# Kernel optimization log

Hardware: AMD Instinct MI355X
Metric: run time of the kernel (lower is better)

The kernel has to match this reference:

```python
import jax, jax.numpy as jnp
import numpy as np

VOCAB, E, H = 64, 256, 1024
B, T = 128, 512
RATE = 0.2  # self.dropout; note: input_dropout on int token ids is a no-op here (see notes)


def _dropout(key, x, rate):
    keep = jax.random.bernoulli(key, 1.0 - rate, x.shape)
    return jnp.where(keep, x / (1.0 - rate), jnp.zeros((), x.dtype))


def _lstm_dir(x, mask, Wx, Wh, b, reverse):
    # x: [B,T,E], mask: [B,T] bool. Keras LSTM gate order i,f,g,o.
    if reverse:
        x = jnp.flip(x, 1)
        mask = jnp.flip(mask, 1)
    xz = jnp.einsum('bte,eg->btg', x, Wx) + b          # [B,T,4H] input projection, one big GEMM
    h0 = jnp.zeros((x.shape[0], Wh.shape[0]), x.dtype)
    c0 = jnp.zeros_like(h0)

    def step(carry, inp):
        h, c = carry
        xz_t, m = inp                                   # [B,4H], [B,1] bool
        z = xz_t + h @ Wh
        i, f, g, o = jnp.split(z, 4, axis=-1)
        c_new = jax.nn.sigmoid(f) * c + jax.nn.sigmoid(i) * jnp.tanh(g)
        h_new = jax.nn.sigmoid(o) * jnp.tanh(c_new)
        h = jnp.where(m, h_new, h)                      # freeze state past row length
        c = jnp.where(m, c_new, c)
        return (h, c), jnp.where(m, h, jnp.zeros((), h.dtype))

    xs = (jnp.swapaxes(xz, 0, 1), jnp.swapaxes(mask, 0, 1)[..., None])
    _, ys = jax.lax.scan(step, (h0, c0), xs)            # ys: [T,B,H]
    ys = jnp.swapaxes(ys, 0, 1)
    if reverse:
        ys = jnp.flip(ys, 1)
    return ys


def setup_inputs() -> dict:
    key = jax.random.key(0)
    ks = jax.random.split(key, 9)
    tokens = jax.random.randint(ks[0], (B, T), 0, VOCAB, dtype=jnp.int32)
    lengths = jax.random.randint(ks[1], (B,), T // 2, T + 1, dtype=jnp.int32)
    emb = jax.random.normal(ks[2], (VOCAB, E), jnp.float32)
    sE, sH = 1.0 / np.sqrt(E), 1.0 / np.sqrt(H)
    Wx_f = jax.random.normal(ks[3], (E, 4 * H), jnp.float32) * sE
    Wh_f = jax.random.normal(ks[4], (H, 4 * H), jnp.float32) * sH
    b_f = jax.random.normal(ks[5], (4 * H,), jnp.float32) * 0.02
    Wx_b = jax.random.normal(ks[6], (E, 4 * H), jnp.float32) * sE
    Wh_b = jax.random.normal(ks[7], (H, 4 * H), jnp.float32) * sH
    b_b = jax.random.normal(ks[8], (4 * H,), jnp.float32) * 0.02
    return {"tokens": tokens, "lengths": lengths, "emb": emb,
            "Wx_f": Wx_f, "Wh_f": Wh_f, "b_f": b_f,
            "Wx_b": Wx_b, "Wh_b": Wh_b, "b_b": b_b}


def reference(tokens, lengths, emb, Wx_f, Wh_f, b_f, Wx_b, Wh_b, b_b):
    mask = jnp.arange(T, dtype=jnp.int32)[None, :] < lengths[:, None]  # [B,T]
    x = jnp.take(emb, tokens, axis=0)                                  # [B,T,E]
    x = _dropout(jax.random.key(1), x, RATE)                           # dropout on embedded
    x = jnp.where(mask[..., None], x, jnp.zeros((), x.dtype))
    out_f = _lstm_dir(x, mask, Wx_f, Wh_f, b_f, reverse=False)
    out_b = _lstm_dir(x, mask, Wx_b, Wh_b, b_b, reverse=True)
    out = out_f + out_b                                                # Bidirectional merge_mode='sum'
    out = _dropout(jax.random.key(2), out, RATE)                       # output dropout
    out = jnp.where(mask[..., None], out, jnp.zeros((), out.dtype))
    return out
```

## Files before the change

kernel.cpp:

```cpp
#include <hip/hip_runtime.h>
#include <hip/hip_bf16.h>

#define B_ 128
#define T_ 512
#define E_ 256
#define H_ 1024
#define G_ 4096
#define KTOT 1280

typedef _Float16 f16x8 __attribute__((ext_vector_type(8)));
typedef float f32x4 __attribute__((ext_vector_type(4)));

__device__ __forceinline__ void threefry2x32(unsigned k0, unsigned k1,
                                             unsigned x0, unsigned x1,
                                             unsigned& o0, unsigned& o1) {
  unsigned k2 = k0 ^ k1 ^ 0x1BD11BDAu;
  unsigned v0 = x0 + k0, v1 = x1 + k1;
#define RND(r) { v0 += v1; v1 = (v1 << (r)) | (v1 >> (32 - (r))); v1 ^= v0; }
  RND(13) RND(15) RND(26) RND(6)   v0 += k1; v1 += k2 + 1u;
  RND(17) RND(29) RND(16) RND(24)  v0 += k2; v1 += k0 + 2u;
  RND(13) RND(15) RND(26) RND(6)   v0 += k0; v1 += k1 + 3u;
  RND(17) RND(29) RND(16) RND(24)  v0 += k1; v1 += k2 + 4u;
  RND(13) RND(15) RND(26) RND(6)   v0 += k2; v1 += k0 + 5u;
#undef RND
  o0 = v0; o1 = v1;
}

__device__ __forceinline__ bool jax_keep(unsigned k1, unsigned i) {
  unsigned o0, o1;
  threefry2x32(0u, k1, 0u, i, o0, o1);
  unsigned bits = o0 ^ o1;
  float u = __uint_as_float((bits >> 9) | 0x3F800000u) - 1.0f;
  return u < 0.8f;
}

__global__ void embed_kernel(const int* __restrict__ tokens,
                             const int* __restrict__ lengths,
                             const float* __restrict__ emb,
                             _Float16* __restrict__ x) {
  unsigned i = blockIdx.x * 256u + threadIdx.x;
  if (i >= (unsigned)(B_ * T_ * E_)) return;
  int e = (int)(i & (E_ - 1));
  int t = (int)((i >> 8) & (T_ - 1));
  int b = (int)(i >> 17);
  int tok = tokens[b * T_ + t];
  float v = emb[tok * E_ + e];
  bool m = t < lengths[b];
  float xv = (m && jax_keep(1u, i)) ? (v * 1.25f) : 0.0f;
  x[i] = (_Float16)xv;
}

__device__ __forceinline__ float sigm(float v) { return 1.0f / (1.0f + __expf(-v)); }
__device__ __forceinline__ float tanh_fast(float v) {
  float c = fminf(fmaxf(v, -10.f), 10.f);
  float e = __expf(2.0f * c);
  return (e - 1.0f) / (e + 1.0f);
}

#define HLD(dst, base, OFF) \
  asm volatile("global_load_dwordx4 %0, %1, off offset:" OFF " sc0 sc1" \
               : "=v"(dst) : "v"(base))
#define HST2(addr, val) \
  asm volatile("global_store_short %0, %1, off sc0 sc1" :: "v"(addr), "v"(val))

#define HEAT() do { \
    _Pragma("unroll") \
    for (int z_ = 0; z_ < 8; ++z_) { \
      hx0 = __builtin_fmaf(hx0, 1.000001f, 1.0f); \
      hx1 = __builtin_fmaf(hx1, 0.999999f, 1.0f); \
    } \
    asm volatile("" :: "v"(hx0), "v"(hx1)); \
  } while (0)

__global__ __launch_bounds__(512) void lstm_kernel(
    const float* __restrict__ WxF, const float* __restrict__ WhF, const float* __restrict__ bF,
    const float* __restrict__ WxB, const float* __restrict__ WhB, const float* __restrict__ bB,
    const int* __restrict__ lengths,
    const _Float16* __restrict__ x,
    _Float16* __restrict__ hbuf,
    unsigned* __restrict__ flags,
    float* __restrict__ out)
{
  __shared__ _Float16 Wl[64 * KTOT];

  const int wg   = blockIdx.x;
  const int dir  = wg & 1;
  const int cb   = wg >> 1;
  const int tid  = (int)threadIdx.x;
  const int lane = tid & 63;
  const int wv   = tid >> 6;

  unsigned* fl_own = flags + dir * 512 + wv * 64;
  unsigned* fl_oth = flags + (dir ^ 1) * 512 + wv * 64;

  const float* Wx = dir ? WxB : WxF;
  const float* Wh = dir ? WhB : WhF;
  const float* bias = dir ? bB : bF;
  _Float16* hb = hbuf + (size_t)dir * (2 * B_ * H_);

  for (int idx = tid; idx < 64 * KTOT; idx += 512) {
    int c = idx & 63, k = idx >> 6;
    int zc = ((c >> 4) << 10) + (cb << 4) + (c & 15);
    float v = (k < E_) ? Wx[k * G_ + zc] : Wh[(k - E_) * G_ + zc];
    Wl[(((k >> 3) << 6) + c) * 8 + (k & 7)] = (_Float16)v;
  }
  __syncthreads();

  const int c0   = lane & 15;
  const int q    = lane >> 4;
  const int ksub = q << 3;
  const int mrow = (wv << 4) + c0;
  const int grow = (wv << 4) + (q << 2);
  const int hc   = (cb << 4) + c0;

  const float b_i = bias[hc], b_f = bias[1024 + hc],
              b_g = bias[2048 + hc], b_o = bias[3072 + hc];
  const int lens[4] = { lengths[grow], lengths[grow + 1],
                        lengths[grow + 2], lengths[grow + 3] };

  const _Float16* xbase = x + (size_t)mrow * T_ * E_;
  const _Float16* wq0 = Wl + (0 * 16 + c0) * 8 + q * 512;
  const _Float16* wq1 = Wl + (1 * 16 + c0) * 8 + q * 512;
  const _Float16* wq2 = Wl + (2 * 16 + c0) * 8 + q * 512;
  const _Float16* wq3 = Wl + (3 * 16 + c0) * 8 + q * 512;

#define MF4(afrag, koff) {                                                              \
    acc0 = __builtin_amdgcn_mfma_f32_16x16x32_f16(afrag, *(const f16x8*)(wq0 + (koff)), acc0, 0, 0, 0); \
    acc1 = __builtin_amdgcn_mfma_f32_16x16x32_f16(afrag, *(const f16x8*)(wq1 + (koff)), acc1, 0, 0, 0); \
    acc2 = __builtin_amdgcn_mfma_f32_16x16x32_f16(afrag, *(const f16x8*)(wq2 + (koff)), acc2, 0, 0, 0); \
    acc3 = __builtin_amdgcn_mfma_f32_16x16x32_f16(afrag, *(const f16x8*)(wq3 + (koff)), acc3, 0, 0, 0); }

  float creg[4] = {0.f, 0.f, 0.f, 0.f}, hreg[4] = {0.f, 0.f, 0.f, 0.f};
  float hx0 = (float)(lane + 1), hx1 = 2.0f;

  int cur = 0;
#pragma unroll 1
  for (int s = 0; s < T_; ++s) {
    const int t = dir ? (T_ - 1 - s) : s;

    if (s == 256) {
      while (1) {
        unsigned f = __hip_atomic_load(fl_oth + lane, __ATOMIC_RELAXED, __HIP_MEMORY_SCOPE_SYSTEM);
        if (__all(f >= 256u)) break;
        HEAT();
      }
      __builtin_amdgcn_fence(__ATOMIC_ACQUIRE, "agent");
    }

    float* op[4];
    float oy[4] = {0.f, 0.f, 0.f, 0.f};
#pragma unroll
    for (int r = 0; r < 4; ++r)
      op[r] = out + ((size_t)(grow + r) * T_ + t) * H_ + hc;
    if (s >= 256) {
#pragma unroll
      for (int r = 0; r < 4; ++r) oy[r] = *op[r];
    }

    f32x4 acc0 = {0.f,0.f,0.f,0.f}, acc1 = {0.f,0.f,0.f,0.f},
          acc2 = {0.f,0.f,0.f,0.f}, acc3 = {0.f,0.f,0.f,0.f};

    {
      const _Float16* xr = xbase + t * E_ + ksub;
#pragma unroll
      for (int kk = 0; kk < 8; ++kk) {
        f16x8 a = *(const f16x8*)(xr + kk * 32);
        MF4(a, kk * 2048);
      }
    }
    __builtin_amdgcn_sched_barrier(0);

    if (s > 0) {
      const unsigned tgt = (unsigned)s;
      while (1) {
        unsigned f = __hip_atomic_load(fl_own + lane, __ATOMIC_RELAXED, __HIP_MEMORY_SCOPE_SYSTEM);
        if (__all(f >= tgt)) break;
        HEAT();
      }
      __builtin_amdgcn_sched_barrier(0);

      const _Float16* hr = hb + (size_t)cur * (B_ * H_) + mrow * H_ + ksub;
      f16x8 ha[32];
      HLD(ha[0],  hr, "0");    HLD(ha[1],  hr, "64");   HLD(ha[2],  hr, "128");  HLD(ha[3],  hr, "192");
      HLD(ha[4],  hr, "256");  HLD(ha[5],  hr, "320");  HLD(ha[6],  hr, "384");  HLD(ha[7],  hr, "448");
      HLD(ha[8],  hr, "512");  HLD(ha[9],  hr, "576");  HLD(ha[10], hr, "640");  HLD(ha[11], hr, "704");
      HLD(ha[12], hr, "768");  HLD(ha[13], hr, "832");  HLD(ha[14], hr, "896");  HLD(ha[15], hr, "960");
      HLD(ha[16], hr, "1024"); HLD(ha[17], hr, "1088"); HLD(ha[18], hr, "1152"); HLD(ha[19], hr, "1216");
      HLD(ha[20], hr, "1280"); HLD(ha[21], hr, "1344"); HLD(ha[22], hr, "1408"); HLD(ha[23], hr, "1472");
      HLD(ha[24], hr, "1536"); HLD(ha[25], hr, "1600"); HLD(ha[26], hr, "1664"); HLD(ha[27], hr, "1728");
      HLD(ha[28], hr, "1792"); HLD(ha[29], hr, "1856"); HLD(ha[30], hr, "1920"); HLD(ha[31], hr, "1984");

      asm volatile("s_waitcnt vmcnt(16)" ::: "memory");
      __builtin_amdgcn_sched_barrier(0);
#pragma unroll
      for (int kk = 0; kk < 16; ++kk) MF4(ha[kk], 16384 + kk * 2048);
      asm volatile("s_waitcnt vmcnt(0)" ::: "memory");
      __builtin_amdgcn_sched_barrier(0);
#pragma unroll
      for (int kk = 16; kk < 32; ++kk) MF4(ha[kk], 16384 + kk * 2048);
    }

    float y[4];
#pragma unroll
    for (int r = 0; r < 4; ++r) {
      bool m = t < lens[r];
      float zi = acc0[r] + b_i;
      float zf = acc1[r] + b_f;
      float zg = acc2[r] + b_g;
      float zo = acc3[r] + b_o;
      float cn = sigm(zf) * creg[r] + sigm(zi) * tanh_fast(zg);
      float hn = sigm(zo) * tanh_fast(cn);
      if (m) { creg[r] = cn; hreg[r] = hn; }
      y[r] = m ? hn : 0.f;
    }

#pragma unroll
    for (int r = 0; r < 4; ++r) {
      _Float16 hf = (_Float16)hreg[r];
      unsigned short hu = *(unsigned short*)&hf;
      _Float16* hw = hb + (size_t)(cur ^ 1) * (B_ * H_) + (grow + r) * H_ + hc;
      HST2(hw, (unsigned)hu);
    }

    if (s == 255) {
#pragma unroll
      for (int r = 0; r < 4; ++r) *op[r] = y[r];
      asm volatile("s_waitcnt vmcnt(0)" ::: "memory");
      if (lane == 0)
        __hip_atomic_store(fl_own + cb, 256u, __ATOMIC_RELEASE, __HIP_MEMORY_SCOPE_SYSTEM);
    } else {
      asm volatile("s_waitcnt vmcnt(0)" ::: "memory");
      if (s < T_ - 1 && lane == 0)
        __hip_atomic_store(fl_own + cb, (unsigned)(s + 1), __ATOMIC_RELAXED, __HIP_MEMORY_SCOPE_SYSTEM);
      if (s < 256) {
#pragma unroll
        for (int r = 0; r < 4; ++r) *op[r] = y[r];
      } else {
#pragma unroll
        for (int r = 0; r < 4; ++r) {
          unsigned i0 = (((unsigned)(grow + r) * T_ + (unsigned)t) << 10) + (unsigned)hc;
          float f0 = oy[r] + y[r];
          *op[r] = jax_keep(2u, i0) ? f0 * 1.25f : 0.f;
        }
      }
    }
    cur ^= 1;
  }
#undef MF4
}

extern "C" void kernel_launch(void* const* d_in, const int* in_sizes, int n_in,
                              void* d_out, int out_size, void* d_ws, size_t ws_size,
                              hipStream_t stream) {
  (void)in_sizes; (void)n_in; (void)out_size; (void)ws_size;
  const int*   tokens  = (const int*)d_in[0];
  const int*   lengths = (const int*)d_in[1];
  const float* emb     = (const float*)d_in[2];
  const float* WxF     = (const float*)d_in[3];
  const float* WhF     = (const float*)d_in[4];
  const float* bF      = (const float*)d_in[5];
  const float* WxB     = (const float*)d_in[6];
  const float* WhB     = (const float*)d_in[7];
  const float* bB      = (const float*)d_in[8];
  float* out = (float*)d_out;

  _Float16* x     = (_Float16*)d_ws;
  _Float16* hbuf  = (_Float16*)((char*)d_ws + (size_t)B_ * T_ * E_ * 2);
  unsigned* flags = (unsigned*)((char*)d_ws + 34603008);

  hipMemsetAsync(flags, 0, 4096, stream);

  embed_kernel<<<(B_ * T_ * E_ + 255) / 256, 256, 0, stream>>>(tokens, lengths, emb, x);

  void* args[] = { (void*)&WxF, (void*)&WhF, (void*)&bF,
                   (void*)&WxB, (void*)&WhB, (void*)&bB,
                   (void*)&lengths, (void*)&x, (void*)&hbuf, (void*)&flags, (void*)&out };
  hipLaunchCooperativeKernel((const void*)lstm_kernel, dim3(128), dim3(512),
                             args, 0, stream);
}
```

Measured before the change: 5.719 ms.

## Route per-step barrier through per-XCC coordinator blocks and cache h loads in L2

Adds one coordinator workgroup per XCC, chosen at runtime from the hardware XCC id. It polls all 128 global step flags and publishes a per-XCC 'go' counter, which worker blocks spin on with s_sleep instead of each wave polling the global flags with busy FMA heating. Workers now signal once per block after __syncthreads, and the separate cross-direction wait at step 256 is folded into the global go condition. The h-state loads drop the sc1 bit so they can be served from the XCC-local L2 after the coordinator's acquire fence. This trades an extra hop of latency per step and reliance on round-robin XCC placement of 136 blocks for less polling traffic and cheaper h reads.

```diff
diff --git a/kernel.cpp b/kernel.cpp
--- a/kernel.cpp
+++ b/kernel.cpp
@@ -7,6 +7,7 @@
 #define H_ 1024
 #define G_ 4096
 #define KTOT 1280
+#define XCC_GETREG_IMM ((31u << 11) | 20u)
 
 typedef _Float16 f16x8 __attribute__((ext_vector_type(8)));
 typedef float f32x4 __attribute__((ext_vector_type(4)));
@@ -57,20 +58,11 @@
   return (e - 1.0f) / (e + 1.0f);
 }
 
-#define HLD(dst, base, OFF) \
-  asm volatile("global_load_dwordx4 %0, %1, off offset:" OFF " sc0 sc1" \
+#define HLDC(dst, base, OFF) \
+  asm volatile("global_load_dwordx4 %0, %1, off offset:" OFF " sc0" \
                : "=v"(dst) : "v"(base))
 #define HST2(addr, val) \
   asm volatile("global_store_short %0, %1, off sc0 sc1" :: "v"(addr), "v"(val))
-
-#define HEAT() do { \
-    _Pragma("unroll") \
-    for (int z_ = 0; z_ < 8; ++z_) { \
-      hx0 = __builtin_fmaf(hx0, 1.000001f, 1.0f); \
-      hx1 = __builtin_fmaf(hx1, 0.999999f, 1.0f); \
-    } \
-    asm volatile("" :: "v"(hx0), "v"(hx1)); \
-  } while (0)
 
 __global__ __launch_bounds__(512) void lstm_kernel(
     const float* __restrict__ WxF, const float* __restrict__ WhF, const float* __restrict__ bF,
@@ -78,20 +70,53 @@
     const int* __restrict__ lengths,
     const _Float16* __restrict__ x,
     _Float16* __restrict__ hbuf,
-    unsigned* __restrict__ flags,
+    unsigned* __restrict__ sync,
     float* __restrict__ out)
 {
   __shared__ _Float16 Wl[64 * KTOT];
 
-  const int wg   = blockIdx.x;
-  const int dir  = wg & 1;
-  const int cb   = wg >> 1;
   const int tid  = (int)threadIdx.x;
   const int lane = tid & 63;
   const int wv   = tid >> 6;
 
-  unsigned* fl_own = flags + dir * 512 + wv * 64;
-  unsigned* fl_oth = flags + (dir ^ 1) * 512 + wv * 64;
+  const unsigned xcc = __builtin_amdgcn_s_getreg(XCC_GETREG_IMM) & 7u;
+  unsigned* flags  = sync;
+  unsigned* roster = sync + 128;
+  unsigned* widctr = sync + 144;
+  unsigned* go     = sync + 256 + xcc * 32;
+
+  if (tid == 0) {
+    unsigned slot = atomicAdd(&roster[xcc], 1u);
+    unsigned wid = 0xFFFFu;
+    if (slot != 0u) wid = atomicAdd(widctr, 1u);
+    ((unsigned*)Wl)[0] = ((slot == 0u) ? 0x80000000u : 0u) | (wid & 0xFFFFu);
+  }
+  __syncthreads();
+  const unsigned pack = ((unsigned*)Wl)[0];
+  __syncthreads();
+  const bool is_coord = (pack >> 31) != 0u;
+  const int  wid      = (int)(pack & 0xFFFFu);
+
+  if (is_coord) {
+    if (wv == 0) {
+      for (unsigned tgt = 1; tgt < (unsigned)T_; ++tgt) {
+        while (1) {
+          unsigned a = __hip_atomic_load(flags + lane,      __ATOMIC_RELAXED, __HIP_MEMORY_SCOPE_SYSTEM);
+          unsigned b = __hip_atomic_load(flags + 64 + lane, __ATOMIC_RELAXED, __HIP_MEMORY_SCOPE_SYSTEM);
+          if (__all(a >= tgt && b >= tgt)) break;
+          __builtin_amdgcn_s_sleep(1);
+        }
+        __builtin_amdgcn_fence(__ATOMIC_ACQUIRE, "agent");
+        if (lane == 0)
+          __hip_atomic_store(go, tgt, __ATOMIC_RELAXED, __HIP_MEMORY_SCOPE_SYSTEM);
+      }
+    }
+    return;
+  }
+  if (wid >= 128) return;
+
+  const int dir = wid & 1;
+  const int cb  = wid >> 1;
 
   const float* Wx = dir ? WxB : WxF;
   const float* Wh = dir ? WhB : WhF;
@@ -131,31 +156,17 @@
     acc3 = __builtin_amdgcn_mfma_f32_16x16x32_f16(afrag, *(const f16x8*)(wq3 + (koff)), acc3, 0, 0, 0); }
 
   float creg[4] = {0.f, 0.f, 0.f, 0.f}, hreg[4] = {0.f, 0.f, 0.f, 0.f};
-  float hx0 = (float)(lane + 1), hx1 = 2.0f;
 
   int cur = 0;
 #pragma unroll 1
   for (int s = 0; s < T_; ++s) {
     const int t = dir ? (T_ - 1 - s) : s;
 
-    if (s == 256) {
-      while (1) {
-        unsigned f = __hip_atomic_load(fl_oth + lane, __ATOMIC_RELAXED, __HIP_MEMORY_SCOPE_SYSTEM);
-        if (__all(f >= 256u)) break;
-        HEAT();
-      }
-      __builtin_amdgcn_fence(__ATOMIC_ACQUIRE, "agent");
-    }
-
     float* op[4];
-    float oy[4] = {0.f, 0.f, 0.f, 0.f};
 #pragma unroll
     for (int r = 0; r < 4; ++r)
       op[r] = out + ((size_t)(grow + r) * T_ + t) * H_ + hc;
-    if (s >= 256) {
-#pragma unroll
-      for (int r = 0; r < 4; ++r) oy[r] = *op[r];
-    }
+    float oy[4] = {0.f, 0.f, 0.f, 0.f};
 
     f32x4 acc0 = {0.f,0.f,0.f,0.f}, acc1 = {0.f,0.f,0.f,0.f},
           acc2 = {0.f,0.f,0.f,0.f}, acc3 = {0.f,0.f,0.f,0.f};
@@ -172,23 +183,25 @@
 
     if (s > 0) {
       const unsigned tgt = (unsigned)s;
-      while (1) {
-        unsigned f = __hip_atomic_load(fl_own + lane, __ATOMIC_RELAXED, __HIP_MEMORY_SCOPE_SYSTEM);
-        if (__all(f >= tgt)) break;
-        HEAT();
-      }
+      while (__hip_atomic_load(go, __ATOMIC_RELAXED, __HIP_MEMORY_SCOPE_AGENT) < tgt)
+        __builtin_amdgcn_s_sleep(1);
       __builtin_amdgcn_sched_barrier(0);
+
+      if (s >= 256) {
+#pragma unroll
+        for (int r = 0; r < 4; ++r) oy[r] = *op[r];
+      }
 
       const _Float16* hr = hb + (size_t)cur * (B_ * H_) + mrow * H_ + ksub;
       f16x8 ha[32];
-      HLD(ha[0],  hr, "0");    HLD(ha[1],  hr, "64");   HLD(ha[2],  hr, "128");  HLD(ha[3],  hr, "192");
-      HLD(ha[4],  hr, "256");  HLD(ha[5],  hr, "320");  HLD(ha[6],  hr, "384");  HLD(ha[7],  hr, "448");
-      HLD(ha[8],  hr, "512");  HLD(ha[9],  hr, "576");  HLD(ha[10], hr, "640");  HLD(ha[11], hr, "704");
-      HLD(ha[12], hr, "768");  HLD(ha[13], hr, "832");  HLD(ha[14], hr, "896");  HLD(ha[15], hr, "960");
-      HLD(ha[16], hr, "1024"); HLD(ha[17], hr, "1088"); HLD(ha[18], hr, "1152"); HLD(ha[19], hr, "1216");
-      HLD(ha[20], hr, "1280"); HLD(ha[21], hr, "1344"); HLD(ha[22], hr, "1408"); HLD(ha[23], hr, "1472");
-      HLD(ha[24], hr, "1536"); HLD(ha[25], hr, "1600"); HLD(ha[26], hr, "1664"); HLD(ha[27], hr, "1728");
-      HLD(ha[28], hr, "1792"); HLD(ha[29], hr, "1856"); HLD(ha[30], hr, "1920"); HLD(ha[31], hr, "1984");
+      HLDC(ha[0],  hr, "0");    HLDC(ha[1],  hr, "64");   HLDC(ha[2],  hr, "128");  HLDC(ha[3],  hr, "192");
+      HLDC(ha[4],  hr, "256");  HLDC(ha[5],  hr, "320");  HLDC(ha[6],  hr, "384");  HLDC(ha[7],  hr, "448");
+      HLDC(ha[8],  hr, "512");  HLDC(ha[9],  hr, "576");  HLDC(ha[10], hr, "640");  HLDC(ha[11], hr, "704");
+      HLDC(ha[12], hr, "768");  HLDC(ha[13], hr, "832");  HLDC(ha[14], hr, "896");  HLDC(ha[15], hr, "960");
+      HLDC(ha[16], hr, "1024"); HLDC(ha[17], hr, "1088"); HLDC(ha[18], hr, "1152"); HLDC(ha[19], hr, "1216");
+      HLDC(ha[20], hr, "1280"); HLDC(ha[21], hr, "1344"); HLDC(ha[22], hr, "1408"); HLDC(ha[23], hr, "1472");
+      HLDC(ha[24], hr, "1536"); HLDC(ha[25], hr, "1600"); HLDC(ha[26], hr, "1664"); HLDC(ha[27], hr, "1728");
+      HLDC(ha[28], hr, "1792"); HLDC(ha[29], hr, "1856"); HLDC(ha[30], hr, "1920"); HLDC(ha[31], hr, "1984");
 
       asm volatile("s_waitcnt vmcnt(16)" ::: "memory");
       __builtin_amdgcn_sched_barrier(0);
@@ -225,13 +238,13 @@
     if (s == 255) {
 #pragma unroll
       for (int r = 0; r < 4; ++r) *op[r] = y[r];
-      asm volatile("s_waitcnt vmcnt(0)" ::: "memory");
-      if (lane == 0)
-        __hip_atomic_store(fl_own + cb, 256u, __ATOMIC_RELEASE, __HIP_MEMORY_SCOPE_SYSTEM);
+      __syncthreads();
+      if (tid == 0)
+        __hip_atomic_store(flags + dir * 64 + cb, 256u, __ATOMIC_RELEASE, __HIP_MEMORY_SCOPE_SYSTEM);
     } else {
-      asm volatile("s_waitcnt vmcnt(0)" ::: "memory");
-      if (s < T_ - 1 && lane == 0)
-        __hip_atomic_store(fl_own + cb, (unsigned)(s + 1), __ATOMIC_RELAXED, __HIP_MEMORY_SCOPE_SYSTEM);
+      __syncthreads();
+      if (tid == 0 && s < T_ - 1)
+        __hip_atomic_store(flags + dir * 64 + cb, (unsigned)(s + 1), __ATOMIC_RELAXED, __HIP_MEMORY_SCOPE_SYSTEM);
       if (s < 256) {
 #pragma unroll
         for (int r = 0; r < 4; ++r) *op[r] = y[r];
@@ -266,15 +279,15 @@
 
   _Float16* x     = (_Float16*)d_ws;
   _Float16* hbuf  = (_Float16*)((char*)d_ws + (size_t)B_ * T_ * E_ * 2);
-  unsigned* flags = (unsigned*)((char*)d_ws + 34603008);
-
-  hipMemsetAsync(flags, 0, 4096, stream);
+  unsigned* sync  = (unsigned*)((char*)d_ws + 34603008);
+
+  hipMemsetAsync(sync, 0, 4096, stream);
 
   embed_kernel<<<(B_ * T_ * E_ + 255) / 256, 256, 0, stream>>>(tokens, lengths, emb, x);
 
   void* args[] = { (void*)&WxF, (void*)&WhF, (void*)&bF,
                    (void*)&WxB, (void*)&WhB, (void*)&bB,
-                   (void*)&lengths, (void*)&x, (void*)&hbuf, (void*)&flags, (void*)&out };
-  hipLaunchCooperativeKernel((const void*)lstm_kernel, dim3(128), dim3(512),
+                   (void*)&lengths, (void*)&x, (void*)&hbuf, (void*)&sync, (void*)&out };
+  hipLaunchCooperativeKernel((const void*)lstm_kernel, dim3(136), dim3(512),
                              args, 0, stream);
 }
```

New measurement: 6.901 ms. 20.7% more time.
